# Kernel tuning notes

Measured on AMD Instinct MI355X. Metric: run time of the kernel, lower is better.

## Reference

```python
import jax, jax.numpy as jnp
import numpy as np

EMBED_DIM = 1024
LATEN_DIM = 1024
B, S = 4, 2048


def setup_inputs() -> dict:
    key = jax.random.key(0)
    k1, k2, k3, k4, k5 = jax.random.split(key, 5)
    xq = jax.random.normal(k1, (B, S, EMBED_DIM), dtype=jnp.float32)
    xk = jax.random.normal(k2, (B, S, EMBED_DIM), dtype=jnp.float32)
    xv = jax.random.normal(k3, (B, S, EMBED_DIM), dtype=jnp.float32)
    # Linear weight init similar to torch default scale
    bound = 1.0 / np.sqrt(EMBED_DIM)
    Wq = jax.random.uniform(k4, (EMBED_DIM, EMBED_DIM), minval=-bound, maxval=bound, dtype=jnp.float32)
    bq = jax.random.uniform(k5, (EMBED_DIM,), minval=-bound, maxval=bound, dtype=jnp.float32)
    # causal mask: 1 => masked (future positions)
    att_mask = jnp.triu(jnp.ones((S, S), dtype=jnp.int32), k=1)
    return {"xq": xq, "xk": xk, "xv": xv, "Wq": Wq, "bq": bq, "att_mask": att_mask}


def reference(xq, xk, xv, Wq, bq, att_mask):
    scale = LATEN_DIM ** (-0.5)
    # Faithful to source: linearQ is applied to all three inputs.
    Q = jnp.einsum('bsd,ed->bse', xq, Wq) + bq
    K = jnp.einsum('bsd,ed->bse', xk, Wq) + bq
    V = jnp.einsum('bsd,ed->bse', xv, Wq) + bq
    scores = jnp.einsum('bqe,bke->bqk', Q, K) * scale  # [B, S, S]
    scores = jnp.where(att_mask == 1, -jnp.inf, scores)
    probs = jax.nn.softmax(scores, axis=-1)
    return jnp.einsum('bqk,bke->bqe', probs, V)
```

## Files before the change

kernel.cpp:

```cpp
#include <hip/hip_runtime.h>
#include <hip/hip_bf16.h>
#include <stdint.h>


typedef __attribute__((ext_vector_type(8))) short bf16x8;
typedef __attribute__((ext_vector_type(4))) float floatx4;

#define DEVI static __device__ __forceinline__

static constexpr int S_ = 2048;
static constexpr int E_ = 1024;
static constexpr int BATCH = 4;
static constexpr int N4X = 8192 * 1024 / 4;

DEVI unsigned short f2b(float f) {
  union { float f; unsigned u; } v; v.f = f;
  return (unsigned short)((v.u + 0x7FFFu + ((v.u >> 16) & 1u)) >> 16);
}

DEVI void async_load16(const void* g, void* l) {
  __builtin_amdgcn_global_load_lds(
      (__attribute__((address_space(1))) void*)(void*)(g),
      (__attribute__((address_space(3))) void*)(l),
      16, 0, 0);
}


DEVI void mfma_tile(const unsigned short* lsA, const unsigned short* lsB,
                    int m0, int n0, int lrow, int lk, floatx4 (&acc)[4][4]) {
  bf16x8 af[4], bfr[4];
#pragma unroll
  for (int i = 0; i < 4; ++i)
    af[i] = *(const bf16x8*)(lsA + (m0 + i * 16 + lrow) * 32 + lk);
#pragma unroll
  for (int i = 0; i < 4; ++i)
    bfr[i] = *(const bf16x8*)(lsB + (n0 + i * 16 + lrow) * 32 + lk);
#pragma unroll
  for (int mi = 0; mi < 4; ++mi)
#pragma unroll
    for (int ni = 0; ni < 4; ++ni)
      acc[mi][ni] = __builtin_amdgcn_mfma_f32_16x16x32_bf16(
          af[mi], bfr[ni], acc[mi][ni], 0, 0, 0);
}

DEVI void stage_bf16(const unsigned short* src, unsigned short* ls, int ld,
                     int tid) {
#pragma unroll
  for (int j = 0; j < 2; ++j) {
    int t = tid + j * 256, row = t >> 2, kk = (t & 3) << 3;
    async_load16(src + (size_t)row * ld + kk, ls + t * 8);
  }
}


template <int ROWS, int NTHR>
DEVI void stage_sw(const unsigned short* __restrict__ src, int ld,
                   unsigned short* ls, int tid) {
#pragma unroll
  for (int j = 0; j < ROWS * 8 / NTHR; ++j) {
    const int u = tid + j * NTHR;
    const int row = u >> 3, slot = u & 7;
    async_load16(src + row * ld + ((slot ^ (row & 7)) << 3), ls + u * 8);
  }
}

DEVI bf16x8 ldfrag(const unsigned short* ls, int r, int kslot) {
  return *(const bf16x8*)(ls + r * 64 + ((kslot ^ (r & 7)) << 3));
}

__global__ void cvt_all(const float* __restrict__ xq,
                        const float* __restrict__ xk,
                        const float* __restrict__ xv,
                        const float* __restrict__ Wq,
                        unsigned short* __restrict__ Xb,
                        unsigned short* __restrict__ Wb) {
  int i = blockIdx.x * blockDim.x + threadIdx.x;
  const float4* src;
  ushort4* dst;
  if (i < 3 * N4X) {
    int seg = i / N4X, off = i - seg * N4X;
    const float* s = (seg == 0) ? xq : (seg == 1) ? xk : xv;
    src = (const float4*)s + off;
    dst = (ushort4*)(Xb + (size_t)seg * 8192 * 1024) + off;
  } else {
    int off = i - 3 * N4X;
    src = (const float4*)Wq + off;
    dst = (ushort4*)Wb + off;
  }
  float4 v = *src;
  ushort4 o;
  o.x = f2b(v.x); o.y = f2b(v.y); o.z = f2b(v.z); o.w = f2b(v.w);
  *dst = o;
}

__global__ __launch_bounds__(256, 2) void gemm_qkv(
    const unsigned short* __restrict__ Xb, const unsigned short* __restrict__ Wb,
    const float* __restrict__ bias, unsigned short* __restrict__ Qb,
    unsigned short* __restrict__ Kb, unsigned short* __restrict__ Vt) {
  __shared__ __align__(16) unsigned short lsA[256 * 64];
  __shared__ __align__(16) unsigned short lsB[128 * 64];
  const int l = blockIdx.x;
  const int xcd = l & 7, i = l >> 3;
  const int bn = i & 7;
  const int bmg = xcd * 12 + (i >> 3);
  const unsigned short* A = Xb + (size_t)bmg * 256 * 1024;
  const unsigned short* W = Wb + (size_t)bn * 128 * 1024;
  const int tid = threadIdx.x;
  const int lane = tid & 63, wave = tid >> 6;
  const int wr = wave >> 1, wc = wave & 1;
  const int lrow = lane & 15, g = lane >> 4;

  floatx4 acc[8][4] = {};
  for (int kt = 0; kt < 16; ++kt) {
    if (kt) __syncthreads();
    stage_sw<256, 256>(A + kt * 64, 1024, lsA, tid);
    stage_sw<128, 256>(W + kt * 64, 1024, lsB, tid);
    __syncthreads();
#pragma unroll
    for (int ks = 0; ks < 2; ++ks) {
      bf16x8 af[8], bfr[4];
#pragma unroll
      for (int mi = 0; mi < 8; ++mi)
        af[mi] = ldfrag(lsA, wr * 128 + mi * 16 + lrow, ks * 4 + g);
#pragma unroll
      for (int ni = 0; ni < 4; ++ni)
        bfr[ni] = ldfrag(lsB, wc * 64 + ni * 16 + lrow, ks * 4 + g);
#pragma unroll
      for (int mi = 0; mi < 8; ++mi)
#pragma unroll
        for (int ni = 0; ni < 4; ++ni)
          acc[mi][ni] = __builtin_amdgcn_mfma_f32_16x16x32_bf16(
              af[mi], bfr[ni], acc[mi][ni], 0, 0, 0);
    }
  }

  const int rb = (lane >> 4) * 4;
  const int input = bmg >> 5;
  unsigned short* C = (input == 0) ? Qb : (input == 1) ? Kb : Vt;
  const int rowbase = (bmg & 31) * 256 + wr * 128;
#pragma unroll
  for (int mi = 0; mi < 8; ++mi)
#pragma unroll
    for (int ni = 0; ni < 4; ++ni) {
      const int gcol = bn * 128 + wc * 64 + ni * 16 + lrow;
      const float bv = bias[gcol];
#pragma unroll
      for (int r = 0; r < 4; ++r) {
        const int grow = rowbase + mi * 16 + rb + r;
        const unsigned short val = f2b(acc[mi][ni][r] + bv);
        if (input == 2) {
          int b = grow >> 11, s = grow & 2047;
          C[((size_t)b * 1024 + gcol) * 2048 + s] = val;
        } else {
          C[(size_t)grow * 1024 + gcol] = val;
        }
      }
    }
}

__global__ __launch_bounds__(256) void gemm_scores_exp(
    const unsigned short* __restrict__ Qb,
    const unsigned short* __restrict__ Kb, unsigned short* __restrict__ P,
    float* __restrict__ lsum) {
  const int l = blockIdx.x;
  const int xcd = l & 7, k = l >> 3;
  const int m = k & 7, gl = k >> 3;
  const int gg = xcd * 12 + gl;
  const int z = gg / 24, r0 = gg % 24;
  const int bm = (r0 < 8) ? r0 : 8 + ((r0 - 8) >> 1);
  const int bn = ((r0 < 8) ? 0 : ((r0 - 8) & 1)) * 8 + m;
  if (bn > bm) return;

  __shared__ __align__(16) unsigned short lsA[2][128 * 32];
  __shared__ __align__(16) unsigned short lsB[2][128 * 32];
  const unsigned short* A = Qb + ((size_t)z * S_ + bm * 128) * E_;
  const unsigned short* Bt = Kb + ((size_t)z * S_ + bn * 128) * E_;
  const int tid = threadIdx.x;
  const int lane = tid & 63, wave = tid >> 6;
  const int m0 = (wave >> 1) * 64, n0 = (wave & 1) * 64;
  const int lrow = lane & 15, lk = (lane >> 4) * 8;

  floatx4 acc[4][4] = {};
  for (int kt = 0; kt < 16; ++kt) {
    if (kt) __syncthreads();
    stage_bf16(A + kt * 64, lsA[0], E_, tid);
    stage_bf16(A + kt * 64 + 32, lsA[1], E_, tid);
    stage_bf16(Bt + kt * 64, lsB[0], E_, tid);
    stage_bf16(Bt + kt * 64 + 32, lsB[1], E_, tid);
    __syncthreads();
    mfma_tile(lsA[0], lsB[0], m0, n0, lrow, lk, acc);
    mfma_tile(lsA[1], lsB[1], m0, n0, lrow, lk, acc);
  }

  const int rb = (lane >> 4) * 4;
  const bool diag = (bm == bn);
#pragma unroll
  for (int mi = 0; mi < 4; ++mi)
#pragma unroll
    for (int r = 0; r < 4; ++r) {
      const int grow = bm * 128 + m0 + mi * 16 + rb + r;
      float rsum = 0.f;
#pragma unroll
      for (int ni = 0; ni < 4; ++ni) {
        const int gcol = bn * 128 + n0 + ni * 16 + lrow;
        float p = __expf(acc[mi][ni][r] * 0.03125f);
        if (diag && gcol > grow) p = 0.f;
        P[((size_t)z * S_ + grow) * S_ + gcol] = f2b(p);
        rsum += p;
      }
#pragma unroll
      for (int off = 1; off < 16; off <<= 1) rsum += __shfl_xor(rsum, off);
      if ((lane & 15) == 0) atomicAdd(&lsum[z * S_ + grow], rsum);
    }
}

__global__ __launch_bounds__(256) void gemm_pv(
    const unsigned short* __restrict__ Pb,
    const unsigned short* __restrict__ Vt, const float* __restrict__ lsum,
    float* __restrict__ Out) {
  __shared__ __align__(16) unsigned short lsA[2][128 * 32];
  __shared__ __align__(16) unsigned short lsB[2][128 * 32];
  const int l = blockIdx.x;
  const int xcd = l & 7, i = l >> 3;
  const int bn = i & 7, j = i >> 3;
  const int z = j >> 1;
  const int bm = (j & 1) ? xcd : 15 - xcd;

  const unsigned short* A = Pb + ((size_t)z * S_ + bm * 128) * S_;
  const unsigned short* Bt = Vt + ((size_t)z * E_ + bn * 128) * S_;
  float* C = Out + (size_t)z * S_ * E_;
  const int tid = threadIdx.x;
  const int lane = tid & 63, wave = tid >> 6;
  const int m0 = (wave >> 1) * 64, n0 = (wave & 1) * 64;
  const int lrow = lane & 15, lk = (lane >> 4) * 8;

  floatx4 acc[4][4] = {};
  const int nKK = (bm + 1) * 2;
  for (int kt = 0; kt < nKK; ++kt) {
    if (kt) __syncthreads();
    stage_bf16(A + kt * 64, lsA[0], S_, tid);
    stage_bf16(A + kt * 64 + 32, lsA[1], S_, tid);
    stage_bf16(Bt + kt * 64, lsB[0], S_, tid);
    stage_bf16(Bt + kt * 64 + 32, lsB[1], S_, tid);
    __syncthreads();
    mfma_tile(lsA[0], lsB[0], m0, n0, lrow, lk, acc);
    mfma_tile(lsA[1], lsB[1], m0, n0, lrow, lk, acc);
  }

  const int rb = (lane >> 4) * 4;
#pragma unroll
  for (int mi = 0; mi < 4; ++mi)
#pragma unroll
    for (int r = 0; r < 4; ++r) {
      const int grow = bm * 128 + m0 + mi * 16 + rb + r;
      const float inv = 1.0f / lsum[z * S_ + grow];
#pragma unroll
      for (int ni = 0; ni < 4; ++ni) {
        const int gcol = bn * 128 + n0 + ni * 16 + lrow;
        C[(size_t)grow * E_ + gcol] = acc[mi][ni][r] * inv;
      }
    }
}

extern "C" void kernel_launch(void* const* d_in, const int* in_sizes, int n_in,
                              void* d_out, int out_size, void* d_ws,
                              size_t ws_size, hipStream_t stream) {
  (void)in_sizes; (void)n_in; (void)out_size; (void)ws_size;
  const float* xq = (const float*)d_in[0];
  const float* xk = (const float*)d_in[1];
  const float* xv = (const float*)d_in[2];
  const float* Wq = (const float*)d_in[3];
  const float* bq = (const float*)d_in[4];
  float* out = (float*)d_out;

  unsigned short* base16 = (unsigned short*)d_ws;
  unsigned short* Xb = base16;
  unsigned short* P = base16;
  unsigned short* Wb = base16 + (size_t)24 * 1024 * 1024;
  unsigned short* Qb = Wb + (size_t)1024 * 1024;
  unsigned short* Kb = Qb + (size_t)8192 * 1024;
  unsigned short* Vt = Kb + (size_t)8192 * 1024;
  float* lsum = (float*)(Vt + (size_t)8192 * 1024);

  hipMemsetAsync(lsum, 0, BATCH * S_ * sizeof(float), stream);

  const int n4tot = 3 * N4X + 1024 * 1024 / 4;
  cvt_all<<<n4tot / 256, 256, 0, stream>>>(xq, xk, xv, Wq, Xb, Wb);

  gemm_qkv<<<768, 256, 0, stream>>>(Xb, Wb, bq, Qb, Kb, Vt);
  gemm_scores_exp<<<768, 256, 0, stream>>>(Qb, Kb, P, lsum);
  gemm_pv<<<512, 256, 0, stream>>>(P, Vt, lsum, out);
}
```

Baseline: 310.1 us.

## Use 256x256 double-buffered 8-wave pipelined k-loop for QKV and scores GEMMs

Result: slower. 350.6 us (+13.0%).

```diff
diff --git a/kernel.cpp b/kernel.cpp
--- a/kernel.cpp
+++ b/kernel.cpp
@@ -25,6 +25,119 @@
       16, 0, 0);
 }
 
+#define BAR asm volatile("s_barrier" ::: "memory")
+#define LGKM0 asm volatile("s_waitcnt lgkmcnt(0)" ::: "memory")
+
+
+DEVI bf16x8 ldfrag64(const unsigned short* ls, int r, int kslot) {
+  return *(const bf16x8*)(ls + r * 64 + ((kslot ^ (r & 7)) << 3));
+}
+
+DEVI void stage_half(const unsigned short* __restrict__ src, int ld,
+                     unsigned short* ls, int tid) {
+#pragma unroll
+  for (int j = 0; j < 2; ++j) {
+    const int u = tid + j * 512;
+    const int row = u >> 3, slot = u & 7;
+    async_load16(src + (size_t)row * ld + ((slot ^ (row & 7)) << 3),
+                 ls + u * 8);
+  }
+}
+
+DEVI void quad16(const bf16x8 (&af)[4][2], const bf16x8 (&bf)[2][2],
+                 floatx4 (&acc)[8][4], int MB, int NB) {
+  __builtin_amdgcn_s_setprio(1);
+#pragma unroll
+  for (int mi = 0; mi < 4; ++mi)
+#pragma unroll
+    for (int ni = 0; ni < 2; ++ni)
+#pragma unroll
+      for (int ks = 0; ks < 2; ++ks)
+        acc[MB + mi][NB + ni] = __builtin_amdgcn_mfma_f32_16x16x32_bf16(
+            af[mi][ks], bf[ni][ks], acc[MB + mi][NB + ni], 0, 0, 0);
+  __builtin_amdgcn_s_setprio(0);
+}
+
+DEVI void kloop256(const unsigned short* __restrict__ A, int lda,
+                   const unsigned short* __restrict__ Bm, int ldb, int NT,
+                   unsigned short* lsA, unsigned short* lsB, int tid,
+                   floatx4 (&acc)[8][4]) {
+  constexpr int SL = 256 * 64;
+  constexpr int HH = 128 * 64;
+  const int lane = tid & 63, g = lane >> 4, lr = lane & 15;
+  const int wr = (tid >> 6) >> 2, wc = (tid >> 6) & 3;
+  const int ar0 = wr * 128 + lr;
+  const int br0 = wc * 64 + lr;
+
+  stage_half(Bm, ldb, lsB, tid);
+  stage_half(A, lda, lsA, tid);
+  stage_half(Bm + (size_t)128 * ldb, ldb, lsB + HH, tid);
+  stage_half(A + (size_t)128 * lda, lda, lsA + HH, tid);
+  if (NT > 1) {
+    stage_half(Bm + 64, ldb, lsB + SL, tid);
+    stage_half(A + 64, lda, lsA + SL, tid);
+    asm volatile("s_waitcnt vmcnt(4)" ::: "memory");
+  } else {
+    asm volatile("s_waitcnt vmcnt(0)" ::: "memory");
+  }
+  BAR;
+
+  bf16x8 a[4][2], b0[2][2], b1[2][2];
+  for (int t = 0; t < NT; ++t) {
+    const int ps = (t & 1) * SL;
+    const int qs = SL - ps;
+    const unsigned short* la = lsA + ps;
+    const unsigned short* lb = lsB + ps;
+#pragma unroll
+    for (int mi = 0; mi < 4; ++mi)
+#pragma unroll
+      for (int ks = 0; ks < 2; ++ks)
+        a[mi][ks] = ldfrag64(la, ar0 + mi * 16, g + ks * 4);
+#pragma unroll
+    for (int ni = 0; ni < 2; ++ni)
+#pragma unroll
+      for (int ks = 0; ks < 2; ++ks)
+        b0[ni][ks] = ldfrag64(lb, br0 + ni * 16, g + ks * 4);
+    if (t + 1 < NT)
+      stage_half(Bm + (size_t)128 * ldb + (t + 1) * 64, ldb, lsB + qs + HH,
+                 tid);
+    BAR; LGKM0;
+    quad16(a, b0, acc, 0, 0);
+    BAR;
+#pragma unroll
+    for (int ni = 0; ni < 2; ++ni)
+#pragma unroll
+      for (int ks = 0; ks < 2; ++ks)
+        b1[ni][ks] = ldfrag64(lb, br0 + 32 + ni * 16, g + ks * 4);
+    if (t + 1 < NT)
+      stage_half(A + (size_t)128 * lda + (t + 1) * 64, lda, lsA + qs + HH,
+                 tid);
+    BAR; LGKM0;
+    quad16(a, b1, acc, 0, 2);
+    BAR;
+#pragma unroll
+    for (int mi = 0; mi < 4; ++mi)
+#pragma unroll
+      for (int ks = 0; ks < 2; ++ks)
+        a[mi][ks] = ldfrag64(la, ar0 + 64 + mi * 16, g + ks * 4);
+    if (t + 2 < NT)
+      stage_half(Bm + (t + 2) * 64, ldb, lsB + ps, tid);
+    BAR; LGKM0;
+    quad16(a, b1, acc, 4, 2);
+    BAR;
+    if (t + 2 < NT)
+      stage_half(A + (t + 2) * 64, lda, lsA + ps, tid);
+    if (t + 2 < NT) {
+      asm volatile("s_waitcnt vmcnt(4)" ::: "memory");
+    } else {
+      asm volatile("s_waitcnt vmcnt(0)" ::: "memory");
+    }
+    BAR;
+    quad16(a, b0, acc, 4, 0);
+    BAR;
+  }
+}
+
 
 DEVI void mfma_tile(const unsigned short* lsA, const unsigned short* lsB,
                     int m0, int n0, int lrow, int lk, floatx4 (&acc)[4][4]) {
@@ -50,22 +163,6 @@
     int t = tid + j * 256, row = t >> 2, kk = (t & 3) << 3;
     async_load16(src + (size_t)row * ld + kk, ls + t * 8);
   }
-}
-
-
-template <int ROWS, int NTHR>
-DEVI void stage_sw(const unsigned short* __restrict__ src, int ld,
-                   unsigned short* ls, int tid) {
-#pragma unroll
-  for (int j = 0; j < ROWS * 8 / NTHR; ++j) {
-    const int u = tid + j * NTHR;
-    const int row = u >> 3, slot = u & 7;
-    async_load16(src + row * ld + ((slot ^ (row & 7)) << 3), ls + u * 8);
-  }
-}
-
-DEVI bf16x8 ldfrag(const unsigned short* ls, int r, int kslot) {
-  return *(const bf16x8*)(ls + r * 64 + ((kslot ^ (r & 7)) << 3));
 }
 
 __global__ void cvt_all(const float* __restrict__ xq,
@@ -93,48 +190,26 @@
   *dst = o;
 }
 
-__global__ __launch_bounds__(256, 2) void gemm_qkv(
+__global__ __launch_bounds__(512, 2) void gemm_qkv(
     const unsigned short* __restrict__ Xb, const unsigned short* __restrict__ Wb,
     const float* __restrict__ bias, unsigned short* __restrict__ Qb,
     unsigned short* __restrict__ Kb, unsigned short* __restrict__ Vt) {
-  __shared__ __align__(16) unsigned short lsA[256 * 64];
-  __shared__ __align__(16) unsigned short lsB[128 * 64];
+  __shared__ __align__(16) unsigned short lsA[2 * 256 * 64];
+  __shared__ __align__(16) unsigned short lsB[2 * 256 * 64];
   const int l = blockIdx.x;
-  const int xcd = l & 7, i = l >> 3;
-  const int bn = i & 7;
-  const int bmg = xcd * 12 + (i >> 3);
+  const int gid = (l & 7) * 48 + (l >> 3);
+  const int bn = gid & 3;
+  const int bmg = gid >> 2;
   const unsigned short* A = Xb + (size_t)bmg * 256 * 1024;
-  const unsigned short* W = Wb + (size_t)bn * 128 * 1024;
+  const unsigned short* W = Wb + (size_t)bn * 256 * 1024;
   const int tid = threadIdx.x;
+
+  floatx4 acc[8][4] = {};
+  kloop256(A, 1024, W, 1024, 16, lsA, lsB, tid, acc);
+
   const int lane = tid & 63, wave = tid >> 6;
-  const int wr = wave >> 1, wc = wave & 1;
-  const int lrow = lane & 15, g = lane >> 4;
-
-  floatx4 acc[8][4] = {};
-  for (int kt = 0; kt < 16; ++kt) {
-    if (kt) __syncthreads();
-    stage_sw<256, 256>(A + kt * 64, 1024, lsA, tid);
-    stage_sw<128, 256>(W + kt * 64, 1024, lsB, tid);
-    __syncthreads();
-#pragma unroll
-    for (int ks = 0; ks < 2; ++ks) {
-      bf16x8 af[8], bfr[4];
-#pragma unroll
-      for (int mi = 0; mi < 8; ++mi)
-        af[mi] = ldfrag(lsA, wr * 128 + mi * 16 + lrow, ks * 4 + g);
-#pragma unroll
-      for (int ni = 0; ni < 4; ++ni)
-        bfr[ni] = ldfrag(lsB, wc * 64 + ni * 16 + lrow, ks * 4 + g);
-#pragma unroll
-      for (int mi = 0; mi < 8; ++mi)
-#pragma unroll
-        for (int ni = 0; ni < 4; ++ni)
-          acc[mi][ni] = __builtin_amdgcn_mfma_f32_16x16x32_bf16(
-              af[mi], bfr[ni], acc[mi][ni], 0, 0, 0);
-    }
-  }
-
-  const int rb = (lane >> 4) * 4;
+  const int wr = wave >> 2, wc = wave & 3;
+  const int lrow = lane & 15, rb = (lane >> 4) * 4;
   const int input = bmg >> 5;
   unsigned short* C = (input == 0) ? Qb : (input == 1) ? Kb : Vt;
   const int rowbase = (bmg & 31) * 256 + wr * 128;
@@ -142,7 +217,7 @@
   for (int mi = 0; mi < 8; ++mi)
 #pragma unroll
     for (int ni = 0; ni < 4; ++ni) {
-      const int gcol = bn * 128 + wc * 64 + ni * 16 + lrow;
+      const int gcol = bn * 256 + wc * 64 + ni * 16 + lrow;
       const float bv = bias[gcol];
 #pragma unroll
       for (int r = 0; r < 4; ++r) {
@@ -158,51 +233,40 @@
     }
 }
 
-__global__ __launch_bounds__(256) void gemm_scores_exp(
+__global__ __launch_bounds__(512, 2) void gemm_scores_exp(
     const unsigned short* __restrict__ Qb,
     const unsigned short* __restrict__ Kb, unsigned short* __restrict__ P,
     float* __restrict__ lsum) {
+  __shared__ __align__(16) unsigned short lsA[2 * 256 * 64];
+  __shared__ __align__(16) unsigned short lsB[2 * 256 * 64];
   const int l = blockIdx.x;
-  const int xcd = l & 7, k = l >> 3;
-  const int m = k & 7, gl = k >> 3;
-  const int gg = xcd * 12 + gl;
-  const int z = gg / 24, r0 = gg % 24;
-  const int bm = (r0 < 8) ? r0 : 8 + ((r0 - 8) >> 1);
-  const int bn = ((r0 < 8) ? 0 : ((r0 - 8) & 1)) * 8 + m;
-  if (bn > bm) return;
-
-  __shared__ __align__(16) unsigned short lsA[2][128 * 32];
-  __shared__ __align__(16) unsigned short lsB[2][128 * 32];
-  const unsigned short* A = Qb + ((size_t)z * S_ + bm * 128) * E_;
-  const unsigned short* Bt = Kb + ((size_t)z * S_ + bn * 128) * E_;
+  const int gid = (l & 7) * 18 + (l >> 3);
+  const int z = gid / 36;
+  int r0 = gid % 36;
+  int bm = 0;
+  for (;;) { const int c = bm + 1; if (r0 < c) break; r0 -= c; ++bm; }
+  const int bnn = r0;
+
+  const unsigned short* A = Qb + ((size_t)z * S_ + bm * 256) * E_;
+  const unsigned short* Bt = Kb + ((size_t)z * S_ + bnn * 256) * E_;
   const int tid = threadIdx.x;
+
+  floatx4 acc[8][4] = {};
+  kloop256(A, E_, Bt, E_, 16, lsA, lsB, tid, acc);
+
   const int lane = tid & 63, wave = tid >> 6;
-  const int m0 = (wave >> 1) * 64, n0 = (wave & 1) * 64;
-  const int lrow = lane & 15, lk = (lane >> 4) * 8;
-
-  floatx4 acc[4][4] = {};
-  for (int kt = 0; kt < 16; ++kt) {
-    if (kt) __syncthreads();
-    stage_bf16(A + kt * 64, lsA[0], E_, tid);
-    stage_bf16(A + kt * 64 + 32, lsA[1], E_, tid);
-    stage_bf16(Bt + kt * 64, lsB[0], E_, tid);
-    stage_bf16(Bt + kt * 64 + 32, lsB[1], E_, tid);
-    __syncthreads();
-    mfma_tile(lsA[0], lsB[0], m0, n0, lrow, lk, acc);
-    mfma_tile(lsA[1], lsB[1], m0, n0, lrow, lk, acc);
-  }
-
-  const int rb = (lane >> 4) * 4;
-  const bool diag = (bm == bn);
-#pragma unroll
-  for (int mi = 0; mi < 4; ++mi)
+  const int wr = wave >> 2, wc = wave & 3;
+  const int lrow = lane & 15, rb = (lane >> 4) * 4;
+  const bool diag = (bnn == bm);
+#pragma unroll
+  for (int mi = 0; mi < 8; ++mi)
 #pragma unroll
     for (int r = 0; r < 4; ++r) {
-      const int grow = bm * 128 + m0 + mi * 16 + rb + r;
+      const int grow = bm * 256 + wr * 128 + mi * 16 + rb + r;
       float rsum = 0.f;
 #pragma unroll
       for (int ni = 0; ni < 4; ++ni) {
-        const int gcol = bn * 128 + n0 + ni * 16 + lrow;
+        const int gcol = bnn * 256 + wc * 64 + ni * 16 + lrow;
         float p = __expf(acc[mi][ni][r] * 0.03125f);
         if (diag && gcol > grow) p = 0.f;
         P[((size_t)z * S_ + grow) * S_ + gcol] = f2b(p);
@@ -287,7 +351,7 @@
   const int n4tot = 3 * N4X + 1024 * 1024 / 4;
   cvt_all<<<n4tot / 256, 256, 0, stream>>>(xq, xk, xv, Wq, Xb, Wb);
 
-  gemm_qkv<<<768, 256, 0, stream>>>(Xb, Wb, bq, Qb, Kb, Vt);
-  gemm_scores_exp<<<768, 256, 0, stream>>>(Qb, Kb, P, lsum);
+  gemm_qkv<<<384, 512, 0, stream>>>(Xb, Wb, bq, Qb, Kb, Vt);
+  gemm_scores_exp<<<144, 512, 0, stream>>>(Qb, Kb, P, lsum);
   gemm_pv<<<512, 256, 0, stream>>>(P, Vt, lsum, out);
 }
```
